# Optimization experiments

Hardware: AMD Instinct MI355X
Metric: run time of the kernel (lower is better)

The kernel has to match this reference:

```python
import jax, jax.numpy as jnp
import numpy as np

B, C, H, W = 4, 64, 64, 64
CQK = C // 8


def setup_inputs() -> dict:
    key = jax.random.key(0)
    k0, k1, k2, k3, k4 = jax.random.split(key, 5)
    x = jax.random.normal(k0, (B, C, H, W), dtype=jnp.float32)
    # Conv1d kernel_size=1, bias=False -> plain [out, in] matmul weights
    Wq = jax.random.normal(k1, (CQK, C), dtype=jnp.float32) * 0.05
    Wk = jax.random.normal(k2, (CQK, C), dtype=jnp.float32) * 0.05
    Wv = jax.random.normal(k3, (C, C), dtype=jnp.float32) * 0.05
    # torch init is 0; use a nonzero scalar so the attention path is exercised
    gamma = jax.random.uniform(k4, (1,), dtype=jnp.float32)
    return {"x": x, "Wq": Wq, "Wk": Wk, "Wv": Wv, "gamma": gamma}


def reference(x, Wq, Wk, Wv, gamma):
    shape = x.shape                      # [B, C, H, W]
    xf = x.reshape(shape[0], shape[1], -1)  # [B, C, N]
    q = jnp.einsum('oc,bcn->bon', Wq, xf)   # [B, C/8, N]
    k = jnp.einsum('oc,bcn->bon', Wk, xf)   # [B, C/8, N]
    v = jnp.einsum('oc,bcn->bon', Wv, xf)   # [B, C, N]
    # score[b, n, m] = sum_c q[b, c, n] * k[b, c, m]  (no 1/sqrt(d) scale)
    score = jnp.einsum('bcn,bcm->bnm', q, k)  # [B, N, N]
    # unconventional softmax over dim=1 (rows/first N axis, i.e. per-column)
    score = jax.nn.softmax(score, axis=1)
    out = jnp.einsum('bcn,bnm->bcm', v, score)  # [B, C, N]
    attention = gamma * out + xf
    return attention.reshape(shape)
```

## Files before the change

kernel.cpp:

```cpp
#include <hip/hip_runtime.h>

#define BB 4
#define NN 4096

typedef __attribute__((ext_vector_type(8))) short short8v;
typedef __attribute__((ext_vector_type(4))) short short4v;
typedef __attribute__((ext_vector_type(4))) float float4v;
typedef __attribute__((ext_vector_type(16))) float f32x16;

__device__ __forceinline__ unsigned short f2bf_rn(float f) {
    unsigned u = __float_as_uint(f);
    u += 0x7FFFu + ((u >> 16) & 1u);
    return (unsigned short)(u >> 16);
}

__global__ __launch_bounds__(512) void qkv_kernel(
    const float* __restrict__ x,
    const float* __restrict__ Wq, const float* __restrict__ Wk,
    const float* __restrict__ Wv,
    unsigned short* __restrict__ Qt, unsigned short* __restrict__ Kt,
    unsigned short* __restrict__ Vsw)
{
    __shared__ __align__(16) unsigned short xs[64][40];
    __shared__ __align__(16) unsigned short Ot[64][40];

    const int t    = threadIdx.x;
    const int w    = t >> 6;
    const int lane = t & 63;
    const int quad = lane >> 4;
    const int l15  = lane & 15;
    const int hi   = lane >> 5;
    const int l31  = lane & 31;
    const int b    = blockIdx.y;
    const int n0   = blockIdx.x * 32;

    const float4v zacc4 = {0.f, 0.f, 0.f, 0.f};

    {
        int c = t >> 3, n4 = (t & 7) * 4;
        float4 xv = *(const float4*)&x[(size_t)(b * 64 + c) * NN + n0 + n4];
        short4v pk;
        pk[0] = (short)f2bf_rn(xv.x); pk[1] = (short)f2bf_rn(xv.y);
        pk[2] = (short)f2bf_rn(xv.z); pk[3] = (short)f2bf_rn(xv.w);
        *(short4v*)&xs[c][n4] = pk;
    }
    __syncthreads();

    #pragma unroll
    for (int ti = 0; ti < 2; ++ti) {
        int ot, nt;
        if (ti == 0) { ot = w >> 1; nt = w & 1; }
        else         { if (w >= 2) break; ot = 4; nt = w; }

        int o = ot * 16 + l15;
        const float* base = (o < 8)  ? (Wq + o * 64)
                           : (o < 16) ? (Wk + (o - 8) * 64)
                                      : (Wv + (o - 16) * 64);
        const float scale = (o < 8) ? 1.4426950408889634f : 1.0f;
        short8v bw0, bw1;
        {
            float4 u0 = *(const float4*)&base[quad * 8];
            float4 u1 = *(const float4*)&base[quad * 8 + 4];
            bw0[0] = (short)f2bf_rn(u0.x * scale); bw0[1] = (short)f2bf_rn(u0.y * scale);
            bw0[2] = (short)f2bf_rn(u0.z * scale); bw0[3] = (short)f2bf_rn(u0.w * scale);
            bw0[4] = (short)f2bf_rn(u1.x * scale); bw0[5] = (short)f2bf_rn(u1.y * scale);
            bw0[6] = (short)f2bf_rn(u1.z * scale); bw0[7] = (short)f2bf_rn(u1.w * scale);
            float4 u2 = *(const float4*)&base[32 + quad * 8];
            float4 u3 = *(const float4*)&base[32 + quad * 8 + 4];
            bw1[0] = (short)f2bf_rn(u2.x * scale); bw1[1] = (short)f2bf_rn(u2.y * scale);
            bw1[2] = (short)f2bf_rn(u2.z * scale); bw1[3] = (short)f2bf_rn(u2.w * scale);
            bw1[4] = (short)f2bf_rn(u3.x * scale); bw1[5] = (short)f2bf_rn(u3.y * scale);
            bw1[6] = (short)f2bf_rn(u3.z * scale); bw1[7] = (short)f2bf_rn(u3.w * scale);
        }

        short8v a0, a1;
        {
            unsigned short* p0 = (unsigned short*)&a0;
            unsigned short* p1 = (unsigned short*)&a1;
            const int nn = nt * 16 + l15;
            #pragma unroll
            for (int j = 0; j < 8; ++j) {
                p0[j] = xs[quad * 8 + j][nn];
                p1[j] = xs[32 + quad * 8 + j][nn];
            }
        }

        float4v d = __builtin_amdgcn_mfma_f32_16x16x32_bf16(a0, bw0, zacc4, 0, 0, 0);
        d = __builtin_amdgcn_mfma_f32_16x16x32_bf16(a1, bw1, d, 0, 0, 0);

        if (ot == 0) {
            #pragma unroll
            for (int r = 0; r < 4; ++r) {
                unsigned short v = f2bf_rn(d[r]);
                size_t n = (size_t)(n0 + nt * 16 + quad * 4 + r);
                if (l15 < 8) Qt[((size_t)b * NN + n) * 8 + l15] = v;
                else         Kt[((size_t)b * NN + n) * 8 + (l15 - 8)] = v;
            }
        } else {
            short4v pk;
            #pragma unroll
            for (int r = 0; r < 4; ++r) pk[r] = (short)f2bf_rn(d[r]);
            *(short4v*)&Ot[(ot - 1) * 16 + l15][nt * 16 + quad * 4] = pk;
        }
    }
    __syncthreads();

    if (w < 4) {
        int ct = w >> 1, nsl = w & 1;
        short8v d = *(const short8v*)&Ot[ct * 32 + l31][nsl * 16 + hi * 8];
        size_t ns = (size_t)blockIdx.x * 2 + nsl;
        unsigned short* cb = Vsw + (((size_t)b * 2 + ct) * 256 + ns) * 512;
        *(short8v*)(cb + lane * 8) = d;
    }
}

__global__ __launch_bounds__(512, 4) void attn_kernel(
    const unsigned short* __restrict__ Qt,
    const unsigned short* __restrict__ Kt,
    const unsigned short* __restrict__ Vsw,
    const float* __restrict__ x, const float* __restrict__ gamma,
    float* __restrict__ out)
{
    __shared__ __align__(16) float Ored[4][64][36];
    __shared__ __align__(16) float Lred[8][32];
    __shared__ __align__(16) float Lf[32];

    const int t    = threadIdx.x;
    const int w    = t >> 6;
    const int lane = t & 63;
    const int hi   = lane >> 5;
    const int l31  = lane & 31;
    const int b    = blockIdx.y;
    const int m0   = blockIdx.x * 32;

    const short8v zfrag = {0, 0, 0, 0, 0, 0, 0, 0};
    const short8v aones = {16256, 16256, 16256, 16256,
                           16256, 16256, 16256, 16256};
    const f32x16 zero16 = {0.f, 0.f, 0.f, 0.f, 0.f, 0.f, 0.f, 0.f,
                           0.f, 0.f, 0.f, 0.f, 0.f, 0.f, 0.f, 0.f};

    short8v bk = zfrag;
    if (!hi) bk = *(const short8v*)(Kt + ((size_t)b * NN + m0 + l31) * 8);

    f32x16 acc0 = zero16, acc1 = zero16, accL = zero16;

    const unsigned short* qp  = Qt + ((size_t)b * NN + w * 512) * 8;
    const unsigned short* v0p = Vsw + ((size_t)b * 2 * 256 + w * 32) * 512 + lane * 8;
    const unsigned short* v1p = v0p + 256 * 512;

    short8v aqn = zfrag;
    if (!hi) aqn = *(const short8v*)(qp + (size_t)l31 * 8);

    for (int it = 0; it < 16; ++it) {
        short8v a00 = *(const short8v*)(v0p + it * 1024);
        short8v a01 = *(const short8v*)(v0p + it * 1024 + 512);
        short8v a10 = *(const short8v*)(v1p + it * 1024);
        short8v a11 = *(const short8v*)(v1p + it * 1024 + 512);

        short8v aq = aqn;

        f32x16 s = __builtin_amdgcn_mfma_f32_32x32x16_bf16(aq, bk, zero16, 0, 0, 0);

        const int itn = (it + 1) & 15;
        if (!hi) aqn = *(const short8v*)(qp + (size_t)(itn * 32 + l31) * 8);

        unsigned xw[8];
        #pragma unroll
        for (int j = 0; j < 8; ++j) {
            float e0 = __builtin_amdgcn_exp2f(s[2 * j]);
            float e1 = __builtin_amdgcn_exp2f(s[2 * j + 1]);
            asm("v_cvt_pk_bf16_f32 %0, %1, %2" : "=v"(xw[j]) : "v"(e0), "v"(e1));
        }

        asm("v_permlane32_swap_b32 %0, %1" : "+v"(xw[2]), "+v"(xw[0]));
        asm("v_permlane32_swap_b32 %0, %1" : "+v"(xw[3]), "+v"(xw[1]));
        asm("v_permlane32_swap_b32 %0, %1" : "+v"(xw[6]), "+v"(xw[4]));
        asm("v_permlane32_swap_b32 %0, %1" : "+v"(xw[7]), "+v"(xw[5]));

        union { unsigned u[4]; short8v v; } bp0, bp1;
        bp0.u[0] = xw[0]; bp0.u[1] = xw[1]; bp0.u[2] = xw[2]; bp0.u[3] = xw[3];
        bp1.u[0] = xw[4]; bp1.u[1] = xw[5]; bp1.u[2] = xw[6]; bp1.u[3] = xw[7];

        __builtin_amdgcn_s_setprio(1);
        acc0 = __builtin_amdgcn_mfma_f32_32x32x16_bf16(a00, bp0.v, acc0, 0, 0, 0);
        acc0 = __builtin_amdgcn_mfma_f32_32x32x16_bf16(a01, bp1.v, acc0, 0, 0, 0);
        acc1 = __builtin_amdgcn_mfma_f32_32x32x16_bf16(a10, bp0.v, acc1, 0, 0, 0);
        acc1 = __builtin_amdgcn_mfma_f32_32x32x16_bf16(a11, bp1.v, acc1, 0, 0, 0);
        accL = __builtin_amdgcn_mfma_f32_32x32x16_bf16(aones, bp0.v, accL, 0, 0, 0);
        accL = __builtin_amdgcn_mfma_f32_32x32x16_bf16(aones, bp1.v, accL, 0, 0, 0);
        __builtin_amdgcn_s_setprio(0);
    }

    if (lane < 32) Lred[w][l31] = accL[0];

    if (w < 4) {
        #pragma unroll
        for (int r = 0; r < 16; ++r) {
            int c = (r & 3) + 8 * (r >> 2) + 4 * hi;
            Ored[w][c][l31]      = acc0[r];
            Ored[w][c + 32][l31] = acc1[r];
        }
    }
    __syncthreads();
    if (w >= 4) {
        #pragma unroll
        for (int r = 0; r < 16; ++r) {
            int c = (r & 3) + 8 * (r >> 2) + 4 * hi;
            Ored[w - 4][c][l31]      += acc0[r];
            Ored[w - 4][c + 32][l31] += acc1[r];
        }
    }
    if (t < 32) {
        float sum = Lred[0][t] + Lred[1][t] + Lred[2][t] + Lred[3][t]
                  + Lred[4][t] + Lred[5][t] + Lred[6][t] + Lred[7][t];
        Lf[t] = 1.f / sum;
    }
    __syncthreads();

    {
        const float gv = gamma[0];
        int c = t >> 3, m4 = (t & 7) * 4;
        float4 o = {0.f, 0.f, 0.f, 0.f};
        #pragma unroll
        for (int k2 = 0; k2 < 4; ++k2) {
            float4 v = *(const float4*)&Ored[k2][c][m4];
            o.x += v.x; o.y += v.y; o.z += v.z; o.w += v.w;
        }
        float4 lf = *(const float4*)&Lf[m4];
        size_t gbase = ((size_t)b * 64 + c) * NN + m0 + m4;
        float4 xv = *(const float4*)&x[gbase];
        float4 r;
        r.x = gv * o.x * lf.x + xv.x;
        r.y = gv * o.y * lf.y + xv.y;
        r.z = gv * o.z * lf.z + xv.z;
        r.w = gv * o.w * lf.w + xv.w;
        *(float4*)&out[gbase] = r;
    }
}

extern "C" void kernel_launch(void* const* d_in, const int* in_sizes, int n_in,
                              void* d_out, int out_size, void* d_ws, size_t ws_size,
                              hipStream_t stream) {
    const float* x     = (const float*)d_in[0];
    const float* Wq    = (const float*)d_in[1];
    const float* Wk    = (const float*)d_in[2];
    const float* Wv    = (const float*)d_in[3];
    const float* gamma = (const float*)d_in[4];
    float* out = (float*)d_out;

    unsigned short* ws = (unsigned short*)d_ws;
    unsigned short* Qt  = ws;
    unsigned short* Kt  = Qt + (size_t)BB * NN * 8;
    unsigned short* Vsw = Kt + (size_t)BB * NN * 8;

    qkv_kernel<<<dim3(NN / 32, BB), 512, 0, stream>>>(x, Wq, Wk, Wv, Qt, Kt, Vsw);
    attn_kernel<<<dim3(NN / 32, BB), 512, 0, stream>>>(Qt, Kt, Vsw, x, gamma, out);
}
```

Baseline: 85.80 us.

## Process 64 output columns per attention block to reuse V and Q loads

Each attention block now handles two 32-column tiles of keys, so every V fragment and Q fragment loaded from global memory feeds twice as many MFMAs. The grid is halved along N, and the shared reduction buffers and epilogue are widened to cover 64 columns. This cuts redundant global reads of V and Q. In exchange it uses more accumulator registers, drops the occupancy hint from 4 to 2 blocks per CU, and leaves only 256 blocks, which lowers parallelism.

```diff
diff --git a/kernel.cpp b/kernel.cpp
--- a/kernel.cpp
+++ b/kernel.cpp
@@ -114,16 +114,16 @@
     }
 }
 
-__global__ __launch_bounds__(512, 4) void attn_kernel(
+__global__ __launch_bounds__(512, 2) void attn_kernel(
     const unsigned short* __restrict__ Qt,
     const unsigned short* __restrict__ Kt,
     const unsigned short* __restrict__ Vsw,
     const float* __restrict__ x, const float* __restrict__ gamma,
     float* __restrict__ out)
 {
-    __shared__ __align__(16) float Ored[4][64][36];
-    __shared__ __align__(16) float Lred[8][32];
-    __shared__ __align__(16) float Lf[32];
+    __shared__ __align__(16) float Ored[4][64][68];
+    __shared__ __align__(16) float Lred[8][2][32];
+    __shared__ __align__(16) float Lf[64];
 
     const int t    = threadIdx.x;
     const int w    = t >> 6;
@@ -131,7 +131,7 @@
     const int hi   = lane >> 5;
     const int l31  = lane & 31;
     const int b    = blockIdx.y;
-    const int m0   = blockIdx.x * 32;
+    const int m0   = blockIdx.x * 64;
 
     const short8v zfrag = {0, 0, 0, 0, 0, 0, 0, 0};
     const short8v aones = {16256, 16256, 16256, 16256,
@@ -139,10 +139,14 @@
     const f32x16 zero16 = {0.f, 0.f, 0.f, 0.f, 0.f, 0.f, 0.f, 0.f,
                            0.f, 0.f, 0.f, 0.f, 0.f, 0.f, 0.f, 0.f};
 
-    short8v bk = zfrag;
-    if (!hi) bk = *(const short8v*)(Kt + ((size_t)b * NN + m0 + l31) * 8);
-
-    f32x16 acc0 = zero16, acc1 = zero16, accL = zero16;
+    short8v bk0 = zfrag, bk1 = zfrag;
+    if (!hi) {
+        bk0 = *(const short8v*)(Kt + ((size_t)b * NN + m0 + l31) * 8);
+        bk1 = *(const short8v*)(Kt + ((size_t)b * NN + m0 + 32 + l31) * 8);
+    }
+
+    f32x16 accA0 = zero16, accA1 = zero16, accB0 = zero16, accB1 = zero16;
+    f32x16 accL0 = zero16, accL1 = zero16;
 
     const unsigned short* qp  = Qt + ((size_t)b * NN + w * 512) * 8;
     const unsigned short* v0p = Vsw + ((size_t)b * 2 * 256 + w * 32) * 512 + lane * 8;
@@ -159,46 +163,69 @@
 
         short8v aq = aqn;
 
-        f32x16 s = __builtin_amdgcn_mfma_f32_32x32x16_bf16(aq, bk, zero16, 0, 0, 0);
+        f32x16 s0 = __builtin_amdgcn_mfma_f32_32x32x16_bf16(aq, bk0, zero16, 0, 0, 0);
+        f32x16 s1 = __builtin_amdgcn_mfma_f32_32x32x16_bf16(aq, bk1, zero16, 0, 0, 0);
 
         const int itn = (it + 1) & 15;
         if (!hi) aqn = *(const short8v*)(qp + (size_t)(itn * 32 + l31) * 8);
 
-        unsigned xw[8];
+        unsigned xw0[8], xw1[8];
         #pragma unroll
         for (int j = 0; j < 8; ++j) {
-            float e0 = __builtin_amdgcn_exp2f(s[2 * j]);
-            float e1 = __builtin_amdgcn_exp2f(s[2 * j + 1]);
-            asm("v_cvt_pk_bf16_f32 %0, %1, %2" : "=v"(xw[j]) : "v"(e0), "v"(e1));
-        }
-
-        asm("v_permlane32_swap_b32 %0, %1" : "+v"(xw[2]), "+v"(xw[0]));
-        asm("v_permlane32_swap_b32 %0, %1" : "+v"(xw[3]), "+v"(xw[1]));
-        asm("v_permlane32_swap_b32 %0, %1" : "+v"(xw[6]), "+v"(xw[4]));
-        asm("v_permlane32_swap_b32 %0, %1" : "+v"(xw[7]), "+v"(xw[5]));
-
-        union { unsigned u[4]; short8v v; } bp0, bp1;
-        bp0.u[0] = xw[0]; bp0.u[1] = xw[1]; bp0.u[2] = xw[2]; bp0.u[3] = xw[3];
-        bp1.u[0] = xw[4]; bp1.u[1] = xw[5]; bp1.u[2] = xw[6]; bp1.u[3] = xw[7];
+            float e0 = __builtin_amdgcn_exp2f(s0[2 * j]);
+            float e1 = __builtin_amdgcn_exp2f(s0[2 * j + 1]);
+            asm("v_cvt_pk_bf16_f32 %0, %1, %2" : "=v"(xw0[j]) : "v"(e0), "v"(e1));
+        }
+        #pragma unroll
+        for (int j = 0; j < 8; ++j) {
+            float e0 = __builtin_amdgcn_exp2f(s1[2 * j]);
+            float e1 = __builtin_amdgcn_exp2f(s1[2 * j + 1]);
+            asm("v_cvt_pk_bf16_f32 %0, %1, %2" : "=v"(xw1[j]) : "v"(e0), "v"(e1));
+        }
+        asm("v_permlane32_swap_b32 %0, %1" : "+v"(xw0[2]), "+v"(xw0[0]));
+        asm("v_permlane32_swap_b32 %0, %1" : "+v"(xw0[3]), "+v"(xw0[1]));
+        asm("v_permlane32_swap_b32 %0, %1" : "+v"(xw0[6]), "+v"(xw0[4]));
+        asm("v_permlane32_swap_b32 %0, %1" : "+v"(xw0[7]), "+v"(xw0[5]));
+        asm("v_permlane32_swap_b32 %0, %1" : "+v"(xw1[2]), "+v"(xw1[0]));
+        asm("v_permlane32_swap_b32 %0, %1" : "+v"(xw1[3]), "+v"(xw1[1]));
+        asm("v_permlane32_swap_b32 %0, %1" : "+v"(xw1[6]), "+v"(xw1[4]));
+        asm("v_permlane32_swap_b32 %0, %1" : "+v"(xw1[7]), "+v"(xw1[5]));
+
+        union { unsigned u[4]; short8v v; } bp00, bp01, bp10, bp11;
+        bp00.u[0] = xw0[0]; bp00.u[1] = xw0[1]; bp00.u[2] = xw0[2]; bp00.u[3] = xw0[3];
+        bp01.u[0] = xw0[4]; bp01.u[1] = xw0[5]; bp01.u[2] = xw0[6]; bp01.u[3] = xw0[7];
+        bp10.u[0] = xw1[0]; bp10.u[1] = xw1[1]; bp10.u[2] = xw1[2]; bp10.u[3] = xw1[3];
+        bp11.u[0] = xw1[4]; bp11.u[1] = xw1[5]; bp11.u[2] = xw1[6]; bp11.u[3] = xw1[7];
 
         __builtin_amdgcn_s_setprio(1);
-        acc0 = __builtin_amdgcn_mfma_f32_32x32x16_bf16(a00, bp0.v, acc0, 0, 0, 0);
-        acc0 = __builtin_amdgcn_mfma_f32_32x32x16_bf16(a01, bp1.v, acc0, 0, 0, 0);
-        acc1 = __builtin_amdgcn_mfma_f32_32x32x16_bf16(a10, bp0.v, acc1, 0, 0, 0);
-        acc1 = __builtin_amdgcn_mfma_f32_32x32x16_bf16(a11, bp1.v, acc1, 0, 0, 0);
-        accL = __builtin_amdgcn_mfma_f32_32x32x16_bf16(aones, bp0.v, accL, 0, 0, 0);
-        accL = __builtin_amdgcn_mfma_f32_32x32x16_bf16(aones, bp1.v, accL, 0, 0, 0);
+        accA0 = __builtin_amdgcn_mfma_f32_32x32x16_bf16(a00, bp00.v, accA0, 0, 0, 0);
+        accA0 = __builtin_amdgcn_mfma_f32_32x32x16_bf16(a01, bp01.v, accA0, 0, 0, 0);
+        accB0 = __builtin_amdgcn_mfma_f32_32x32x16_bf16(a10, bp00.v, accB0, 0, 0, 0);
+        accB0 = __builtin_amdgcn_mfma_f32_32x32x16_bf16(a11, bp01.v, accB0, 0, 0, 0);
+        accA1 = __builtin_amdgcn_mfma_f32_32x32x16_bf16(a00, bp10.v, accA1, 0, 0, 0);
+        accA1 = __builtin_amdgcn_mfma_f32_32x32x16_bf16(a01, bp11.v, accA1, 0, 0, 0);
+        accB1 = __builtin_amdgcn_mfma_f32_32x32x16_bf16(a10, bp10.v, accB1, 0, 0, 0);
+        accB1 = __builtin_amdgcn_mfma_f32_32x32x16_bf16(a11, bp11.v, accB1, 0, 0, 0);
+        accL0 = __builtin_amdgcn_mfma_f32_32x32x16_bf16(aones, bp00.v, accL0, 0, 0, 0);
+        accL0 = __builtin_amdgcn_mfma_f32_32x32x16_bf16(aones, bp01.v, accL0, 0, 0, 0);
+        accL1 = __builtin_amdgcn_mfma_f32_32x32x16_bf16(aones, bp10.v, accL1, 0, 0, 0);
+        accL1 = __builtin_amdgcn_mfma_f32_32x32x16_bf16(aones, bp11.v, accL1, 0, 0, 0);
         __builtin_amdgcn_s_setprio(0);
     }
 
-    if (lane < 32) Lred[w][l31] = accL[0];
+    if (lane < 32) {
+        Lred[w][0][l31] = accL0[0];
+        Lred[w][1][l31] = accL1[0];
+    }
 
     if (w < 4) {
         #pragma unroll
         for (int r = 0; r < 16; ++r) {
             int c = (r & 3) + 8 * (r >> 2) + 4 * hi;
-            Ored[w][c][l31]      = acc0[r];
-            Ored[w][c + 32][l31] = acc1[r];
+            Ored[w][c][l31]           = accA0[r];
+            Ored[w][c][32 + l31]      = accA1[r];
+            Ored[w][c + 32][l31]      = accB0[r];
+            Ored[w][c + 32][32 + l31] = accB1[r];
         }
     }
     __syncthreads();
@@ -206,35 +233,42 @@
         #pragma unroll
         for (int r = 0; r < 16; ++r) {
             int c = (r & 3) + 8 * (r >> 2) + 4 * hi;
-            Ored[w - 4][c][l31]      += acc0[r];
-            Ored[w - 4][c + 32][l31] += acc1[r];
-        }
-    }
-    if (t < 32) {
-        float sum = Lred[0][t] + Lred[1][t] + Lred[2][t] + Lred[3][t]
-                  + Lred[4][t] + Lred[5][t] + Lred[6][t] + Lred[7][t];
+            Ored[w - 4][c][l31]           += accA0[r];
+            Ored[w - 4][c][32 + l31]      += accA1[r];
+            Ored[w - 4][c + 32][l31]      += accB0[r];
+            Ored[w - 4][c + 32][32 + l31] += accB1[r];
+        }
+    }
+    if (t < 64) {
+        int mt = t >> 5, m = t & 31;
+        float sum = Lred[0][mt][m] + Lred[1][mt][m] + Lred[2][mt][m] + Lred[3][mt][m]
+                  + Lred[4][mt][m] + Lred[5][mt][m] + Lred[6][mt][m] + Lred[7][mt][m];
         Lf[t] = 1.f / sum;
     }
     __syncthreads();
 
     {
         const float gv = gamma[0];
-        int c = t >> 3, m4 = (t & 7) * 4;
-        float4 o = {0.f, 0.f, 0.f, 0.f};
-        #pragma unroll
-        for (int k2 = 0; k2 < 4; ++k2) {
-            float4 v = *(const float4*)&Ored[k2][c][m4];
-            o.x += v.x; o.y += v.y; o.z += v.z; o.w += v.w;
-        }
-        float4 lf = *(const float4*)&Lf[m4];
-        size_t gbase = ((size_t)b * 64 + c) * NN + m0 + m4;
-        float4 xv = *(const float4*)&x[gbase];
-        float4 r;
-        r.x = gv * o.x * lf.x + xv.x;
-        r.y = gv * o.y * lf.y + xv.y;
-        r.z = gv * o.z * lf.z + xv.z;
-        r.w = gv * o.w * lf.w + xv.w;
-        *(float4*)&out[gbase] = r;
+        int c = t >> 3, m8 = (t & 7) * 8;
+        #pragma unroll
+        for (int h = 0; h < 2; ++h) {
+            int m4 = m8 + h * 4;
+            float4 o = {0.f, 0.f, 0.f, 0.f};
+            #pragma unroll
+            for (int k2 = 0; k2 < 4; ++k2) {
+                float4 v = *(const float4*)&Ored[k2][c][m4];
+                o.x += v.x; o.y += v.y; o.z += v.z; o.w += v.w;
+            }
+            float4 lf = *(const float4*)&Lf[m4];
+            size_t gbase = ((size_t)b * 64 + c) * NN + m0 + m4;
+            float4 xv = *(const float4*)&x[gbase];
+            float4 r;
+            r.x = gv * o.x * lf.x + xv.x;
+            r.y = gv * o.y * lf.y + xv.y;
+            r.z = gv * o.z * lf.z + xv.z;
+            r.w = gv * o.w * lf.w + xv.w;
+            *(float4*)&out[gbase] = r;
+        }
     }
 }
 
@@ -254,5 +288,5 @@
     unsigned short* Vsw = Kt + (size_t)BB * NN * 8;
 
     qkv_kernel<<<dim3(NN / 32, BB), 512, 0, stream>>>(x, Wq, Wk, Wv, Qt, Kt, Vsw);
-    attn_kernel<<<dim3(NN / 32, BB), 512, 0, stream>>>(Qt, Kt, Vsw, x, gamma, out);
-}
+    attn_kernel<<<dim3(NN / 64, BB), 512, 0, stream>>>(Qt, Kt, Vsw, x, gamma, out);
+}
```

Result: no change. 84.20 us (-1.9%).
